# Kernel tuning notes

Hardware: AMD Instinct MI355X
Metric: run time of the kernel (lower is better)

## Reference

```python
import jax, jax.numpy as jnp
import numpy as np

B, S, D = 2, 2048, 2048
HQ, HKV = 16, 4
HD = D // HQ            # 128
NREP = HQ // HKV        # 4
FF = 8192
NEG = -1e9


def setup_inputs() -> dict:
    key = jax.random.key(0)
    ks = jax.random.split(key, 12)
    w = lambda k, shp: (jax.random.normal(k, shp, jnp.float32) * 0.02)
    causal = jnp.where(jnp.tril(jnp.ones((S, S), bool)), 0.0, NEG).astype(jnp.float32)
    return {
        "x": jax.random.normal(ks[0], (B, S, D), jnp.float32),
        "mask": causal[None, None],                       # [1,1,S,S] additive
        "pos_bias": w(ks[1], (HQ, S, S)),                  # learned additive bias per head
        "wq": w(ks[2], (D, D)),
        "wk": w(ks[3], (D, HKV * HD)),
        "wv": w(ks[4], (D, HKV * HD)),
        "wo": w(ks[5], (D, D)),
        "attn_norm_w": jnp.ones((D,), jnp.float32),
        "linear_norm_w": jnp.ones((D,), jnp.float32),
        "gate_w": w(ks[6], (D, FF)),
        "gate_b": jnp.zeros((FF,), jnp.float32),
        "lin_w": w(ks[7], (D, FF)),
        "lin_b": jnp.zeros((FF,), jnp.float32),
        "out_w": w(ks[8], (FF, D)),
        "out_b": jnp.zeros((D,), jnp.float32),
    }


def rmsnorm(x, w, eps=1e-6):
    return x * jax.lax.rsqrt(jnp.mean(x * x, -1, keepdims=True) + eps) * w


def reference(x, mask, pos_bias, wq, wk, wv, wo, attn_norm_w, linear_norm_w,
              gate_w, gate_b, lin_w, lin_b, out_w, out_b):
    # --- attention block ---
    xn = rmsnorm(x, attn_norm_w)
    # q grouped: head h = g*NREP + r (matches torch repeat_interleave on kv heads)
    q = (xn @ wq).reshape(B, S, HKV, NREP, HD)             # [B,S,G,R,Hd]
    k = (xn @ wk).reshape(B, S, HKV, HD)                    # [B,S,G,Hd]
    v = (xn @ wv).reshape(B, S, HKV, HD)
    scores = jnp.einsum('bqgrd,bkgd->bgrqk', q, k) / np.sqrt(HD).astype(np.float32)
    scores = scores + pos_bias.reshape(HKV, NREP, S, S)[None]
    scores = scores + mask[:, :, None]                       # broadcast [1,1,1,S,S]
    attn = jax.nn.softmax(scores, axis=-1)
    o = jnp.einsum('bgrqk,bkgd->bqgrd', attn, v).reshape(B, S, D)
    a = x + o @ wo
    # --- SwiGLU FFN block ---
    an = rmsnorm(a, linear_norm_w)
    h = jax.nn.silu(an @ lin_w + lin_b) * (an @ gate_w + gate_b)
    return a + (h @ out_w + out_b)
```

## Files before the change

### kernel.cpp

```cpp
#include <hip/hip_runtime.h>
#include <hip/hip_bf16.h>

using bf16x8 = __attribute__((ext_vector_type(8))) __bf16;
using f32x4  = __attribute__((ext_vector_type(4))) float;

constexpr int Bc = 2, Sc = 2048, Dc = 2048, HQc = 16, HKVc = 4, HDc = 128, FFc = 8192;

__device__ __forceinline__ void gload16(const void* g, void* l) {
  __builtin_amdgcn_global_load_lds((const __attribute__((address_space(1))) void*)g,
                                   (__attribute__((address_space(3))) void*)l, 16, 0, 0);
}

__global__ __launch_bounds__(256) void wtrans_kernel(const float* __restrict__ in,
                                                     __bf16* __restrict__ out,
                                                     int R, int C) {
  __shared__ float tile[32][33];
  const int tx = threadIdx.x, ty = threadIdx.y;
  const int c0 = blockIdx.x * 32, r0 = blockIdx.y * 32;
#pragma unroll
  for (int i = 0; i < 4; ++i)
    tile[ty + 8 * i][tx] = in[(size_t)(r0 + ty + 8 * i) * C + (c0 + tx)];
  __syncthreads();
#pragma unroll
  for (int i = 0; i < 4; ++i)
    out[(size_t)(c0 + ty + 8 * i) * R + (r0 + tx)] = (__bf16)tile[tx][ty + 8 * i];
}

__global__ __launch_bounds__(256) void vtrans_kernel(const __bf16* __restrict__ V,
                                                     __bf16* __restrict__ Vt, int stride) {
  __shared__ __bf16 tile[32][33];
  const int tx = threadIdx.x, ty = threadIdx.y;
  const int s0 = blockIdx.x * 32, c0 = blockIdx.y * 32, b = blockIdx.z;
#pragma unroll
  for (int i = 0; i < 4; ++i)
    tile[ty + 8 * i][tx] = V[(size_t)(b * Sc + s0 + ty + 8 * i) * stride + c0 + tx];
  __syncthreads();
#pragma unroll
  for (int i = 0; i < 4; ++i) {
    const int c = c0 + ty + 8 * i;
    Vt[((size_t)(b * HKVc + (c >> 7)) * HDc + (c & 127)) * Sc + s0 + tx] = tile[tx][ty + 8 * i];
  }
}

__global__ __launch_bounds__(256) void rmsnorm_kernel(const float* __restrict__ x,
                                                      const float* __restrict__ w,
                                                      __bf16* __restrict__ out) {
  const int row = blockIdx.x;
  const int t = threadIdx.x;
  const float* xr = x + (size_t)row * Dc + t * 8;
  float4 v0 = *(const float4*)(xr);
  float4 v1 = *(const float4*)(xr + 4);
  float ss = v0.x * v0.x + v0.y * v0.y + v0.z * v0.z + v0.w * v0.w +
             v1.x * v1.x + v1.y * v1.y + v1.z * v1.z + v1.w * v1.w;
#pragma unroll
  for (int off = 32; off > 0; off >>= 1) ss += __shfl_down(ss, off);
  __shared__ float wsum[4];
  if ((t & 63) == 0) wsum[t >> 6] = ss;
  __syncthreads();
  const float tot = wsum[0] + wsum[1] + wsum[2] + wsum[3];
  const float scale = rsqrtf(tot * (1.0f / Dc) + 1e-6f);
  const float* wp = w + t * 8;
  bf16x8 o;
  o[0] = (__bf16)(v0.x * scale * wp[0]);
  o[1] = (__bf16)(v0.y * scale * wp[1]);
  o[2] = (__bf16)(v0.z * scale * wp[2]);
  o[3] = (__bf16)(v0.w * scale * wp[3]);
  o[4] = (__bf16)(v1.x * scale * wp[4]);
  o[5] = (__bf16)(v1.y * scale * wp[5]);
  o[6] = (__bf16)(v1.z * scale * wp[6]);
  o[7] = (__bf16)(v1.w * scale * wp[7]);
  *(bf16x8*)(out + (size_t)row * Dc + t * 8) = o;
}

__global__ __launch_bounds__(256) void reduce_out_kernel(const float* __restrict__ p0,
                                                         const float* __restrict__ p1,
                                                         const float* __restrict__ res,
                                                         const float* __restrict__ bias,
                                                         float* __restrict__ out) {
  const size_t i = ((size_t)blockIdx.x * 256 + threadIdx.x) * 4;
  const int col = (int)(i & 2047);
  float4 a = *(const float4*)(p0 + i);
  float4 b = *(const float4*)(p1 + i);
  float4 r = *(const float4*)(res + i);
  float4 bs = *(const float4*)(bias + col);
  float4 o;
  o.x = a.x + b.x + r.x + bs.x;
  o.y = a.y + b.y + r.y + bs.y;
  o.z = a.z + b.z + r.z + bs.z;
  o.w = a.w + b.w + r.w + bs.w;
  *(float4*)(out + i) = o;
}

template <int EP>
__global__ __launch_bounds__(512, 2) void gemm256(
    const __bf16* __restrict__ A, const __bf16* __restrict__ Bt,
    void* __restrict__ Cout, int M, int N, int K, int lda,
    const float* __restrict__ res, const float* __restrict__ bias,
    const __bf16* aux) {
  __shared__ __attribute__((aligned(16))) __bf16 lds[65536];
  const int tid = threadIdx.x;
  const int l = tid & 63, w = tid >> 6;
  const int lm = l & 15, lh = l >> 4;
  const int wr = w >> 2, wc = w & 3;

  int wg = blockIdx.y * gridDim.x + blockIdx.x;
  const int nwg = gridDim.x * gridDim.y;
  wg = (wg & 7) * (nwg >> 3) + (wg >> 3);
  const int bm = (wg / gridDim.x) * 256, bn = (wg % gridDim.x) * 256;
  const int kz = blockIdx.z;

  f32x4 acc[8][4] = {};

  const int srow = w * 16 + (l >> 2);
  const int scol = (((l & 3) ^ ((l >> 3) & 3))) * 8;
  const __bf16* abase = A + (size_t)(bm + srow) * lda + kz * K + scol;
  const __bf16* bbase = Bt + (size_t)(bn + srow) * lda + kz * K + scol;
  const size_t j1 = (size_t)128 * lda;
  const int sdst = w * 512;

  const int xsw = (lm >> 1) & 3;
  const int aoff = (wr * 128 + lm) * 32 + (lh ^ xsw) * 8;
  const int boff = (wc * 64 + lm) * 32 + (lh ^ xsw) * 8;
  const int NT = K >> 6;

  gload16(abase, &lds[sdst]);
  gload16(abase + j1, &lds[4096 + sdst]);
  gload16(bbase, &lds[32768 + sdst]);
  gload16(bbase + j1, &lds[32768 + 4096 + sdst]);
  gload16(abase + 32, &lds[8192 + sdst]);
  gload16(abase + 32 + j1, &lds[8192 + 4096 + sdst]);
  gload16(bbase + 32, &lds[32768 + 8192 + sdst]);
  gload16(bbase + 32 + j1, &lds[32768 + 8192 + 4096 + sdst]);
  gload16(abase + 64, &lds[16384 + sdst]);
  gload16(abase + 64 + j1, &lds[16384 + 4096 + sdst]);
  gload16(bbase + 64, &lds[32768 + 16384 + sdst]);
  gload16(bbase + 64 + j1, &lds[32768 + 16384 + 4096 + sdst]);
  asm volatile("s_waitcnt vmcnt(4)" ::: "memory");
  __builtin_amdgcn_s_barrier();
  __builtin_amdgcn_sched_barrier(0);

  bf16x8 bq[4];
  for (int t = 0; t < NT; ++t) {
    const int pb = (t & 1) * 16384;
    const int qb = 16384 - pb;

    {
      bf16x8 af[4];
#pragma unroll
      for (int i = 0; i < 4; ++i) af[i] = *(const bf16x8*)&lds[pb + aoff + i * 512];
#pragma unroll
      for (int n = 0; n < 4; ++n) bq[n] = *(const bf16x8*)&lds[32768 + pb + boff + n * 512];
      if (t + 1 < NT) {
        const __bf16* s = abase + (size_t)(t + 1) * 64 + 32;
        gload16(s, &lds[qb + 8192 + sdst]);
        gload16(s + j1, &lds[qb + 8192 + 4096 + sdst]);
      }
      __builtin_amdgcn_s_barrier();
      __builtin_amdgcn_s_setprio(1);
#pragma unroll
      for (int m = 0; m < 4; ++m)
#pragma unroll
        for (int n = 0; n < 4; ++n)
          acc[m][n] = __builtin_amdgcn_mfma_f32_16x16x32_bf16(af[m], bq[n], acc[m][n], 0, 0, 0);
      __builtin_amdgcn_s_setprio(0);
      __builtin_amdgcn_s_barrier();
    }
    {
      bf16x8 af[4];
#pragma unroll
      for (int i = 0; i < 4; ++i) af[i] = *(const bf16x8*)&lds[pb + aoff + 2048 + i * 512];
      if (t + 1 < NT) {
        const __bf16* s = bbase + (size_t)(t + 1) * 64 + 32;
        gload16(s, &lds[32768 + qb + 8192 + sdst]);
        gload16(s + j1, &lds[32768 + qb + 8192 + 4096 + sdst]);
      }
      __builtin_amdgcn_s_barrier();
      __builtin_amdgcn_s_setprio(1);
#pragma unroll
      for (int m = 0; m < 4; ++m)
#pragma unroll
        for (int n = 0; n < 4; ++n)
          acc[m + 4][n] = __builtin_amdgcn_mfma_f32_16x16x32_bf16(af[m], bq[n], acc[m + 4][n], 0, 0, 0);
      __builtin_amdgcn_s_setprio(0);
      __builtin_amdgcn_s_barrier();
    }
    {
      bf16x8 af[4];
#pragma unroll
      for (int i = 0; i < 4; ++i) af[i] = *(const bf16x8*)&lds[pb + 8192 + aoff + i * 512];
#pragma unroll
      for (int n = 0; n < 4; ++n) bq[n] = *(const bf16x8*)&lds[32768 + pb + 8192 + boff + n * 512];
      if (t + 2 < NT) {
        const __bf16* s = abase + (size_t)(t + 2) * 64;
        gload16(s, &lds[pb + sdst]);
        gload16(s + j1, &lds[pb + 4096 + sdst]);
      }
      __builtin_amdgcn_s_barrier();
      __builtin_amdgcn_s_setprio(1);
#pragma unroll
      for (int m = 0; m < 4; ++m)
#pragma unroll
        for (int n = 0; n < 4; ++n)
          acc[m][n] = __builtin_amdgcn_mfma_f32_16x16x32_bf16(af[m], bq[n], acc[m][n], 0, 0, 0);
      __builtin_amdgcn_s_setprio(0);
      __builtin_amdgcn_s_barrier();
    }
    {
      bf16x8 af[4];
#pragma unroll
      for (int i = 0; i < 4; ++i)
        af[i] = *(const bf16x8*)&lds[pb + 8192 + aoff + 2048 + i * 512];
      if (t + 2 < NT) {
        const __bf16* s = bbase + (size_t)(t + 2) * 64;
        gload16(s, &lds[32768 + pb + sdst]);
        gload16(s + j1, &lds[32768 + pb + 4096 + sdst]);
        asm volatile("s_waitcnt vmcnt(4)" ::: "memory");
      } else {
        asm volatile("s_waitcnt vmcnt(0)" ::: "memory");
      }
      __builtin_amdgcn_sched_barrier(0);
      __builtin_amdgcn_s_barrier();
      __builtin_amdgcn_s_setprio(1);
#pragma unroll
      for (int m = 0; m < 4; ++m)
#pragma unroll
        for (int n = 0; n < 4; ++n)
          acc[m + 4][n] = __builtin_amdgcn_mfma_f32_16x16x32_bf16(af[m], bq[n], acc[m + 4][n], 0, 0, 0);
      __builtin_amdgcn_s_setprio(0);
      __builtin_amdgcn_s_barrier();
    }
  }

#pragma unroll
  for (int m = 0; m < 8; ++m) {
#pragma unroll
    for (int n = 0; n < 4; ++n) {
#pragma unroll
      for (int r = 0; r < 4; ++r) {
        const int row = bm + wr * 128 + m * 16 + lh * 4 + r;
        const int col = bn + wc * 64 + n * 16 + lm;
        const size_t idx = (size_t)row * N + col;
        const float v = acc[m][n][r];
        if constexpr (EP == 0) {
          ((__bf16*)Cout)[idx] = (__bf16)v;
        } else if constexpr (EP == 1) {
          ((float*)Cout)[idx] = v + res[idx];
        } else if constexpr (EP == 2) {
          ((__bf16*)Cout)[idx] = (__bf16)(v + bias[col]);
        } else if constexpr (EP == 3) {
          const float tt = v + bias[col];
          const float sil = tt / (1.0f + __expf(-tt));
          ((__bf16*)Cout)[idx] = (__bf16)(sil * (float)aux[idx]);
        } else if constexpr (EP == 4) {
          ((float*)Cout)[idx] = res[idx] + v + bias[col];
        } else {
          ((float*)Cout)[(size_t)kz * M * N + idx] = v;
        }
      }
    }
  }
}

__global__ __launch_bounds__(512) void attn_kernel(
    const __bf16* __restrict__ QKV, const __bf16* __restrict__ Vt,
    const float* __restrict__ pbias, __bf16* __restrict__ O) {
  __shared__ __bf16 klds[64][136];
  __shared__ __bf16 vlds[128][72];
  __shared__ __bf16 plds[8][16][72];
  const int tid = threadIdx.x;
  const int w = tid >> 6, l = tid & 63;
  const int lm = l & 15, lh = l >> 4;
  const int by = blockIdx.x;
  const int b = by >> 4, h = by & 15;
  const int g = h >> 2;
  const int qy = blockIdx.y;
  const int qt = (qy < 8) ? qy : (23 - qy);
  const int q0b = qt * 128;
  const int q0 = q0b + w * 16;

  bf16x8 qf[4];
  {
    const __bf16* qbase = QKV + (size_t)(b * Sc + q0 + lm) * 3072 + h * HDc + lh * 8;
#pragma unroll
    for (int ks = 0; ks < 4; ++ks) qf[ks] = *(const bf16x8*)(qbase + ks * 32);
  }

  f32x4 oacc[8] = {};
  float mrow[4] = {-3e38f, -3e38f, -3e38f, -3e38f};
  float lrow[4] = {0.f, 0.f, 0.f, 0.f};
  const float sc_qk = 0.088388347648318447f;

  const __bf16* kgb = QKV + (size_t)b * Sc * 3072 + 2048 + g * 128;
  const __bf16* vgb = Vt + (size_t)(b * HKVc + g) * HDc * Sc;
  const float* pgb = pbias + (size_t)h * Sc * Sc;

  const int skr = tid >> 4;
  const int skc = (tid & 15) * 8;
  const int svr = tid >> 3;
  const int svc = (tid & 7) * 8;

  bf16x8 kreg[2], vreg[2];
  float breg[4][4];

  {
#pragma unroll
    for (int i = 0; i < 2; ++i)
      kreg[i] = *(const bf16x8*)(kgb + (size_t)(i * 32 + skr) * 3072 + skc);
#pragma unroll
    for (int i = 0; i < 2; ++i)
      vreg[i] = *(const bf16x8*)(vgb + (size_t)(i * 64 + svr) * Sc + svc);
#pragma unroll
    for (int c = 0; c < 4; ++c)
#pragma unroll
      for (int r = 0; r < 4; ++r)
        breg[c][r] = pgb[(size_t)(q0 + lh * 4 + r) * Sc + c * 16 + lm];
  }

  const int nt = 2 * qt + 2;
  for (int t = 0; t < nt; ++t) {
    const int kv0 = t * 64;
    __syncthreads();
#pragma unroll
    for (int i = 0; i < 2; ++i) *(bf16x8*)&klds[i * 32 + skr][skc] = kreg[i];
#pragma unroll
    for (int i = 0; i < 2; ++i) *(bf16x8*)&vlds[i * 64 + svr][svc] = vreg[i];
    __syncthreads();

    if (t + 1 < nt) {
      const int nv0 = kv0 + 64;
#pragma unroll
      for (int i = 0; i < 2; ++i)
        kreg[i] = *(const bf16x8*)(kgb + (size_t)(nv0 + i * 32 + skr) * 3072 + skc);
#pragma unroll
      for (int i = 0; i < 2; ++i)
        vreg[i] = *(const bf16x8*)(vgb + (size_t)(i * 64 + svr) * Sc + nv0 + svc);
    }

    float sv[4][4];
#pragma unroll
    for (int c = 0; c < 4; ++c) {
      f32x4 acc = {};
#pragma unroll
      for (int ks = 0; ks < 4; ++ks) {
        bf16x8 kf = *(const bf16x8*)&klds[c * 16 + lm][ks * 32 + lh * 8];
        acc = __builtin_amdgcn_mfma_f32_16x16x32_bf16(qf[ks], kf, acc, 0, 0, 0);
      }
      const int kvg = kv0 + c * 16 + lm;
#pragma unroll
      for (int r = 0; r < 4; ++r) {
        const int qg = q0 + lh * 4 + r;
        sv[c][r] = (kvg <= qg) ? (acc[r] * sc_qk + breg[c][r]) : -1e9f;
      }
    }

    if (t + 1 < nt) {
      const int nv0 = kv0 + 64;
#pragma unroll
      for (int c = 0; c < 4; ++c)
#pragma unroll
        for (int r = 0; r < 4; ++r)
          breg[c][r] = pgb[(size_t)(q0 + lh * 4 + r) * Sc + nv0 + c * 16 + lm];
    }

    float tmv[4];
    bool needb = false;
#pragma unroll
    for (int r = 0; r < 4; ++r) {
      float tm = fmaxf(fmaxf(sv[0][r], sv[1][r]), fmaxf(sv[2][r], sv[3][r]));
      tm = fmaxf(tm, __shfl_xor(tm, 1));
      tm = fmaxf(tm, __shfl_xor(tm, 2));
      tm = fmaxf(tm, __shfl_xor(tm, 4));
      tm = fmaxf(tm, __shfl_xor(tm, 8));
      tmv[r] = tm;
      needb = needb || (tm > mrow[r] + 8.0f);
    }
    if (__any(needb)) {
#pragma unroll
      for (int r = 0; r < 4; ++r) {
        const float mn = fmaxf(mrow[r], tmv[r]);
        const float fac = __expf(mrow[r] - mn);
        mrow[r] = mn;
        lrow[r] *= fac;
#pragma unroll
        for (int d0 = 0; d0 < 8; ++d0) oacc[d0][r] *= fac;
      }
    }
    float pv[4][4];
#pragma unroll
    for (int r = 0; r < 4; ++r) {
      float rs = 0.f;
#pragma unroll
      for (int c = 0; c < 4; ++c) {
        pv[c][r] = __expf(sv[c][r] - mrow[r]);
        rs += pv[c][r];
      }
      rs += __shfl_xor(rs, 1);
      rs += __shfl_xor(rs, 2);
      rs += __shfl_xor(rs, 4);
      rs += __shfl_xor(rs, 8);
      lrow[r] += rs;
    }

#pragma unroll
    for (int c = 0; c < 4; ++c)
#pragma unroll
      for (int r = 0; r < 4; ++r)
        plds[w][lh * 4 + r][c * 16 + lm] = (__bf16)pv[c][r];
    asm volatile("s_waitcnt lgkmcnt(0)" ::: "memory");
    __builtin_amdgcn_sched_barrier(0);
    bf16x8 pa0 = *(const bf16x8*)&plds[w][lm][lh * 8];
    bf16x8 pa1 = *(const bf16x8*)&plds[w][lm][32 + lh * 8];
#pragma unroll
    for (int d0 = 0; d0 < 8; ++d0) {
      bf16x8 vf0 = *(const bf16x8*)&vlds[d0 * 16 + lm][lh * 8];
      bf16x8 vf1 = *(const bf16x8*)&vlds[d0 * 16 + lm][32 + lh * 8];
      oacc[d0] = __builtin_amdgcn_mfma_f32_16x16x32_bf16(pa0, vf0, oacc[d0], 0, 0, 0);
      oacc[d0] = __builtin_amdgcn_mfma_f32_16x16x32_bf16(pa1, vf1, oacc[d0], 0, 0, 0);
    }
  }

  __syncthreads();
  if (w < 4) {
#pragma unroll
    for (int r = 0; r < 4; ++r) {
      const float inv = 1.0f / lrow[r];
#pragma unroll
      for (int d0 = 0; d0 < 8; ++d0)
        klds[w * 16 + lh * 4 + r][d0 * 16 + lm] = (__bf16)(oacc[d0][r] * inv);
    }
    asm volatile("s_waitcnt lgkmcnt(0)" ::: "memory");
    __builtin_amdgcn_sched_barrier(0);
    __bf16* ob = O + ((size_t)(b * Sc + q0 + lm) * HQc + h) * HDc;
#pragma unroll
    for (int c = 0; c < 4; ++c)
      *(bf16x8*)(ob + (c * 4 + lh) * 8) = *(const bf16x8*)&klds[w * 16 + lm][(c * 4 + lh) * 8];
  }
  __syncthreads();
  if (w >= 4) {
    const int wl = w - 4;
#pragma unroll
    for (int r = 0; r < 4; ++r) {
      const float inv = 1.0f / lrow[r];
#pragma unroll
      for (int d0 = 0; d0 < 8; ++d0)
        klds[wl * 16 + lh * 4 + r][d0 * 16 + lm] = (__bf16)(oacc[d0][r] * inv);
    }
    asm volatile("s_waitcnt lgkmcnt(0)" ::: "memory");
    __builtin_amdgcn_sched_barrier(0);
    __bf16* ob = O + ((size_t)(b * Sc + q0 + lm) * HQc + h) * HDc;
#pragma unroll
    for (int c = 0; c < 4; ++c)
      *(bf16x8*)(ob + (c * 4 + lh) * 8) = *(const bf16x8*)&klds[wl * 16 + lm][(c * 4 + lh) * 8];
  }
}

extern "C" void kernel_launch(void* const* d_in, const int* in_sizes, int n_in,
                              void* d_out, int out_size, void* d_ws, size_t ws_size,
                              hipStream_t stream) {
  const float* x = (const float*)d_in[0];
  const float* pbias = (const float*)d_in[2];
  const float* wq = (const float*)d_in[3];
  const float* wk = (const float*)d_in[4];
  const float* wv = (const float*)d_in[5];
  const float* wo = (const float*)d_in[6];
  const float* attn_norm_w = (const float*)d_in[7];
  const float* linear_norm_w = (const float*)d_in[8];
  const float* gate_w = (const float*)d_in[9];
  const float* gate_b = (const float*)d_in[10];
  const float* lin_w = (const float*)d_in[11];
  const float* lin_b = (const float*)d_in[12];
  const float* out_w = (const float*)d_in[13];
  const float* out_b = (const float*)d_in[14];

  if (ws_size < 335544320) return;

  char* ws = (char*)d_ws;
  __bf16* wqkvt = (__bf16*)(ws + 0);
  __bf16* wot = (__bf16*)(ws + 12582912);
  __bf16* gatewt = (__bf16*)(ws + 20971520);
  __bf16* linwt = (__bf16*)(ws + 54525952);
  __bf16* outwt = (__bf16*)(ws + 88080384);
  __bf16* xn = (__bf16*)(ws + 121634816);
  __bf16* QKV = (__bf16*)(ws + 138412032);
  __bf16* Vtb = (__bf16*)(ws + 163577856);
  float* abuf = (float*)(ws + 167772160);
  __bf16* hbuf = (__bf16*)(ws + 201326592);
  float* psum = (float*)(ws + 268435456);
  __bf16* Ob = xn;
  __bf16* an = QKV;

  const dim3 tb(32, 8);
  wtrans_kernel<<<dim3(64, 64), tb, 0, stream>>>(wq, wqkvt, 2048, 2048);
  wtrans_kernel<<<dim3(16, 64), tb, 0, stream>>>(wk, wqkvt + (size_t)2048 * 2048, 2048, 512);
  wtrans_kernel<<<dim3(16, 64), tb, 0, stream>>>(wv, wqkvt + (size_t)2560 * 2048, 2048, 512);
  wtrans_kernel<<<dim3(64, 64), tb, 0, stream>>>(wo, wot, 2048, 2048);
  wtrans_kernel<<<dim3(256, 64), tb, 0, stream>>>(gate_w, gatewt, 2048, 8192);
  wtrans_kernel<<<dim3(256, 64), tb, 0, stream>>>(lin_w, linwt, 2048, 8192);
  wtrans_kernel<<<dim3(64, 256), tb, 0, stream>>>(out_w, outwt, 8192, 2048);

  rmsnorm_kernel<<<4096, 256, 0, stream>>>(x, attn_norm_w, xn);

  gemm256<0><<<dim3(12, 16), 512, 0, stream>>>(xn, wqkvt, QKV, 4096, 3072, 2048, 2048, nullptr, nullptr, nullptr);

  vtrans_kernel<<<dim3(64, 16, 2), tb, 0, stream>>>(QKV + 2560, Vtb, 3072);

  attn_kernel<<<dim3(32, 16), 512, 0, stream>>>(QKV, Vtb, pbias, Ob);

  gemm256<1><<<dim3(8, 16), 512, 0, stream>>>(Ob, wot, abuf, 4096, 2048, 2048, 2048, x, nullptr, nullptr);

  rmsnorm_kernel<<<4096, 256, 0, stream>>>(abuf, linear_norm_w, an);

  gemm256<2><<<dim3(32, 16), 512, 0, stream>>>(an, gatewt, hbuf, 4096, 8192, 2048, 2048, nullptr, gate_b, nullptr);
  gemm256<3><<<dim3(32, 16), 512, 0, stream>>>(an, linwt, hbuf, 4096, 8192, 2048, 2048, nullptr, lin_b, hbuf);

  gemm256<5><<<dim3(8, 16, 2), 512, 0, stream>>>(hbuf, outwt, psum, 4096, 2048, 4096, 8192, nullptr, nullptr, nullptr);
  reduce_out_kernel<<<8192, 256, 0, stream>>>(psum, psum + (size_t)4096 * 2048, abuf, out_b, (float*)d_out);
}
```

Measured before the change: 821.4 us.

## Fuse gate and linear FFN GEMMs into one dual-B SwiGLU kernel

```diff
diff --git a/kernel.cpp b/kernel.cpp
--- a/kernel.cpp
+++ b/kernel.cpp
@@ -103,10 +103,10 @@
   const int lm = l & 15, lh = l >> 4;
   const int wr = w >> 2, wc = w & 3;
 
-  int wg = blockIdx.y * gridDim.x + blockIdx.x;
+  int wg = blockIdx.x * gridDim.y + blockIdx.y;
   const int nwg = gridDim.x * gridDim.y;
   wg = (wg & 7) * (nwg >> 3) + (wg >> 3);
-  const int bm = (wg / gridDim.x) * 256, bn = (wg % gridDim.x) * 256;
+  const int bm = (wg % gridDim.y) * 256, bn = (wg / gridDim.y) * 256;
   const int kz = blockIdx.z;
 
   f32x4 acc[8][4] = {};
@@ -245,17 +245,170 @@
           ((__bf16*)Cout)[idx] = (__bf16)v;
         } else if constexpr (EP == 1) {
           ((float*)Cout)[idx] = v + res[idx];
-        } else if constexpr (EP == 2) {
-          ((__bf16*)Cout)[idx] = (__bf16)(v + bias[col]);
-        } else if constexpr (EP == 3) {
-          const float tt = v + bias[col];
-          const float sil = tt / (1.0f + __expf(-tt));
-          ((__bf16*)Cout)[idx] = (__bf16)(sil * (float)aux[idx]);
-        } else if constexpr (EP == 4) {
-          ((float*)Cout)[idx] = res[idx] + v + bias[col];
         } else {
           ((float*)Cout)[(size_t)kz * M * N + idx] = v;
         }
+      }
+    }
+  }
+}
+
+__global__ __launch_bounds__(512, 2) void gemmffn(
+    const __bf16* __restrict__ A, const __bf16* __restrict__ Bg,
+    const __bf16* __restrict__ Bl, __bf16* __restrict__ H,
+    const float* __restrict__ gb, const float* __restrict__ lb) {
+  __shared__ __attribute__((aligned(16))) __bf16 lds[73728];
+  const int tid = threadIdx.x;
+  const int l = tid & 63, w = tid >> 6;
+  const int lm = l & 15, lh = l >> 4;
+  const int wr = w >> 2, wc = w & 3;
+
+  int wg = blockIdx.x * 32 + blockIdx.y;
+  wg = (wg & 7) * 128 + (wg >> 3);
+  const int bm = (wg & 31) * 128;
+  const int bn = (wg >> 5) * 256;
+
+  f32x4 ag[4][4] = {}, al[4][4] = {};
+
+  const int srA = tid >> 2;
+  const int scA = ((tid & 3) ^ ((tid >> 3) & 3)) * 8;
+  const __bf16* abase = A + (size_t)(bm + srA) * 2048 + scA;
+  const int srB = w * 16 + (l >> 2);
+  const int scB = (((l & 3) ^ ((l >> 3) & 3))) * 8;
+  const __bf16* gbase = Bg + (size_t)(bn + srB) * 2048 + scB;
+  const __bf16* lbase = Bl + (size_t)(bn + srB) * 2048 + scB;
+  const size_t j1 = (size_t)128 * 2048;
+  const int sdst = w * 512;
+
+  const int xsw = (lm >> 1) & 3;
+  const int aro = (wr * 64 + lm) * 32 + (lh ^ xsw) * 8;
+  const int bro = (wc * 64 + lm) * 32 + (lh ^ xsw) * 8;
+  const int NT = 32;
+
+  gload16(abase, &lds[sdst]);
+  gload16(abase + 32, &lds[4096 + sdst]);
+  gload16(gbase, &lds[8192 + sdst]);
+  gload16(gbase + j1, &lds[8192 + 4096 + sdst]);
+  gload16(gbase + 32, &lds[8192 + 8192 + sdst]);
+  gload16(gbase + 32 + j1, &lds[8192 + 8192 + 4096 + sdst]);
+  gload16(lbase, &lds[40960 + sdst]);
+  gload16(lbase + j1, &lds[40960 + 4096 + sdst]);
+  gload16(lbase + 32, &lds[40960 + 8192 + sdst]);
+  gload16(lbase + 32 + j1, &lds[40960 + 8192 + 4096 + sdst]);
+  gload16(gbase + 64, &lds[8192 + 16384 + sdst]);
+  gload16(gbase + 64 + j1, &lds[8192 + 16384 + 4096 + sdst]);
+  gload16(lbase + 64, &lds[40960 + 16384 + sdst]);
+  gload16(lbase + 64 + j1, &lds[40960 + 16384 + 4096 + sdst]);
+  asm volatile("s_waitcnt vmcnt(4)" ::: "memory");
+  __builtin_amdgcn_s_barrier();
+  __builtin_amdgcn_sched_barrier(0);
+
+  for (int t = 0; t < NT; ++t) {
+    const int gB = 8192 + (t & 1) * 16384;
+    const int lB = 40960 + (t & 1) * 16384;
+    const int gBn = 8192 + 16384 - (t & 1) * 16384;
+    const int lBn = 40960 + 16384 - (t & 1) * 16384;
+
+    bf16x8 a0[4], a1[4], bq[4];
+    {
+#pragma unroll
+      for (int i = 0; i < 4; ++i) a0[i] = *(const bf16x8*)&lds[aro + i * 512];
+#pragma unroll
+      for (int i = 0; i < 4; ++i) a1[i] = *(const bf16x8*)&lds[4096 + aro + i * 512];
+#pragma unroll
+      for (int n = 0; n < 4; ++n) bq[n] = *(const bf16x8*)&lds[gB + bro + n * 512];
+      if (t + 1 < NT) {
+        const __bf16* s = gbase + (size_t)(t + 1) * 64 + 32;
+        gload16(s, &lds[gBn + 8192 + sdst]);
+        gload16(s + j1, &lds[gBn + 8192 + 4096 + sdst]);
+      }
+      __builtin_amdgcn_s_barrier();
+      __builtin_amdgcn_s_setprio(1);
+#pragma unroll
+      for (int m = 0; m < 4; ++m)
+#pragma unroll
+        for (int n = 0; n < 4; ++n)
+          ag[m][n] = __builtin_amdgcn_mfma_f32_16x16x32_bf16(a0[m], bq[n], ag[m][n], 0, 0, 0);
+      __builtin_amdgcn_s_setprio(0);
+      __builtin_amdgcn_s_barrier();
+    }
+    {
+#pragma unroll
+      for (int n = 0; n < 4; ++n) bq[n] = *(const bf16x8*)&lds[lB + bro + n * 512];
+      if (t + 1 < NT) {
+        const __bf16* s = lbase + (size_t)(t + 1) * 64 + 32;
+        gload16(s, &lds[lBn + 8192 + sdst]);
+        gload16(s + j1, &lds[lBn + 8192 + 4096 + sdst]);
+      }
+      __builtin_amdgcn_s_barrier();
+      __builtin_amdgcn_s_setprio(1);
+#pragma unroll
+      for (int m = 0; m < 4; ++m)
+#pragma unroll
+        for (int n = 0; n < 4; ++n)
+          al[m][n] = __builtin_amdgcn_mfma_f32_16x16x32_bf16(a0[m], bq[n], al[m][n], 0, 0, 0);
+      __builtin_amdgcn_s_setprio(0);
+      __builtin_amdgcn_s_barrier();
+    }
+    {
+#pragma unroll
+      for (int n = 0; n < 4; ++n) bq[n] = *(const bf16x8*)&lds[gB + 8192 + bro + n * 512];
+      if (t + 1 < NT) {
+        const __bf16* sa = abase + (size_t)(t + 1) * 64;
+        gload16(sa, &lds[sdst]);
+        gload16(sa + 32, &lds[4096 + sdst]);
+      }
+      if (t + 2 < NT) {
+        const __bf16* s = gbase + (size_t)(t + 2) * 64;
+        gload16(s, &lds[gB + sdst]);
+        gload16(s + j1, &lds[gB + 4096 + sdst]);
+      }
+      __builtin_amdgcn_s_barrier();
+      __builtin_amdgcn_s_setprio(1);
+#pragma unroll
+      for (int m = 0; m < 4; ++m)
+#pragma unroll
+        for (int n = 0; n < 4; ++n)
+          ag[m][n] = __builtin_amdgcn_mfma_f32_16x16x32_bf16(a1[m], bq[n], ag[m][n], 0, 0, 0);
+      __builtin_amdgcn_s_setprio(0);
+      __builtin_amdgcn_s_barrier();
+    }
+    {
+#pragma unroll
+      for (int n = 0; n < 4; ++n) bq[n] = *(const bf16x8*)&lds[lB + 8192 + bro + n * 512];
+      if (t + 2 < NT) {
+        const __bf16* s = lbase + (size_t)(t + 2) * 64;
+        gload16(s, &lds[lB + sdst]);
+        gload16(s + j1, &lds[lB + 4096 + sdst]);
+        asm volatile("s_waitcnt vmcnt(4)" ::: "memory");
+      } else {
+        asm volatile("s_waitcnt vmcnt(0)" ::: "memory");
+      }
+      __builtin_amdgcn_sched_barrier(0);
+      __builtin_amdgcn_s_barrier();
+      __builtin_amdgcn_s_setprio(1);
+#pragma unroll
+      for (int m = 0; m < 4; ++m)
+#pragma unroll
+        for (int n = 0; n < 4; ++n)
+          al[m][n] = __builtin_amdgcn_mfma_f32_16x16x32_bf16(a1[m], bq[n], al[m][n], 0, 0, 0);
+      __builtin_amdgcn_s_setprio(0);
+      __builtin_amdgcn_s_barrier();
+    }
+  }
+
+#pragma unroll
+  for (int m = 0; m < 4; ++m) {
+#pragma unroll
+    for (int n = 0; n < 4; ++n) {
+#pragma unroll
+      for (int r = 0; r < 4; ++r) {
+        const int row = bm + wr * 64 + m * 16 + lh * 4 + r;
+        const int col = bn + wc * 64 + n * 16 + lm;
+        const float g = ag[m][n][r] + gb[col];
+        const float li = al[m][n][r] + lb[col];
+        const float sil = li / (1.0f + __expf(-li));
+        H[(size_t)row * 8192 + col] = (__bf16)(sil * g);
       }
     }
   }
@@ -510,8 +663,7 @@
 
   rmsnorm_kernel<<<4096, 256, 0, stream>>>(abuf, linear_norm_w, an);
 
-  gemm256<2><<<dim3(32, 16), 512, 0, stream>>>(an, gatewt, hbuf, 4096, 8192, 2048, 2048, nullptr, gate_b, nullptr);
-  gemm256<3><<<dim3(32, 16), 512, 0, stream>>>(an, linwt, hbuf, 4096, 8192, 2048, 2048, nullptr, lin_b, hbuf);
+  gemmffn<<<dim3(32, 32), 512, 0, stream>>>(an, gatewt, linwt, hbuf, gate_b, lin_b);
 
   gemm256<5><<<dim3(8, 16, 2), 512, 0, stream>>>(hbuf, outwt, psum, 4096, 2048, 4096, 8192, nullptr, nullptr, nullptr);
   reduce_out_kernel<<<8192, 256, 0, stream>>>(psum, psum + (size_t)4096 * 2048, abuf, out_b, (float*)d_out);
```

Result: no change. 833.7 us (+1.5%).
